# Performance work log

Hardware: AMD Instinct MI355X
Metric: run time of the kernel (lower is better)

The kernel has to match this reference:

```python
import jax, jax.numpy as jnp
import numpy as np

B, T, D, U = 16, 1600, 512, 1024


def setup_inputs() -> dict:
    key = jax.random.key(0)
    ks = jax.random.split(key, 7)
    sk = 1.0 / np.sqrt(D)
    sr = 1.0 / np.sqrt(U)
    return {
        "x": jax.random.normal(ks[0], (B, T, D), jnp.float32),
        "x_len": jnp.full((B,), T, dtype=jnp.int32),
        "kernel_f": jax.random.normal(ks[1], (D, 4 * U), jnp.float32) * sk,
        "rkernel_f": jax.random.normal(ks[2], (U, 4 * U), jnp.float32) * sr,
        "bias_f": jnp.zeros((4 * U,), jnp.float32),
        "kernel_b": jax.random.normal(ks[3], (D, 4 * U), jnp.float32) * sk,
        "rkernel_b": jax.random.normal(ks[4], (U, 4 * U), jnp.float32) * sr,
        "bias_b": jnp.zeros((4 * U,), jnp.float32),
    }


def _lstm(x, kernel, rkernel, bias):
    """Keras-semantics LSTM, return_sequences=True. x: [B,T,D] -> [B,T,U]."""
    units = rkernel.shape[0]
    # precompute input projection for all timesteps (the big GEMM)
    xg = jnp.einsum('btd,dg->btg', x, kernel) + bias  # [B,T,4U]
    xg = jnp.swapaxes(xg, 0, 1)  # [T,B,4U] for scan
    h0 = jnp.zeros((x.shape[0], units), x.dtype)
    c0 = jnp.zeros((x.shape[0], units), x.dtype)

    def step(carry, g_in):
        h, c = carry
        g = g_in + h @ rkernel  # [B,4U]
        i, f, cc, o = jnp.split(g, 4, axis=-1)  # Keras gate order i,f,c,o
        c = jax.nn.sigmoid(f) * c + jax.nn.sigmoid(i) * jnp.tanh(cc)
        h = jax.nn.sigmoid(o) * jnp.tanh(c)
        return (h, c), h

    _, hs = jax.lax.scan(step, (h0, c0), xg)  # hs: [T,B,U]
    return jnp.swapaxes(hs, 0, 1)


def reference(x, x_len, kernel_f, rkernel_f, bias_f, kernel_b, rkernel_b, bias_b):
    # Bidirectional(LSTM(units, return_sequences=True)), merge_mode='concat'
    out_f = _lstm(x, kernel_f, rkernel_f, bias_f)
    out_b = _lstm(x[:, ::-1], kernel_b, rkernel_b, bias_b)[:, ::-1]
    outputs = jnp.concatenate([out_f, out_b], axis=-1)  # [B,T,2U]
    return outputs, x_len
```

## Files before the change

kernel.cpp:

```cpp
#include <hip/hip_runtime.h>

#define B_   16
#define T_   1600
#define D_   512
#define U_   1024
#define G_   4096
#define NWG  256
#define TPB  256
#define KTOT 1536
#define APAD 1544
#define ROWB (APAD*2)
#define X16OFF (1 << 18)

typedef __attribute__((ext_vector_type(8))) __bf16 bf16x8;
typedef __attribute__((ext_vector_type(4))) float  f32x4;
typedef __attribute__((ext_vector_type(2))) float  f32x2;
typedef __attribute__((ext_vector_type(8))) unsigned short us8v;
typedef unsigned long long u64;

__device__ __forceinline__ unsigned short f2bf(float f) {
  unsigned u = __builtin_bit_cast(unsigned, f);
  u += 0x7FFFu + ((u >> 16) & 1u);
  return (unsigned short)(u >> 16);
}
__device__ __forceinline__ bf16x8 cvt8(const float4 a, const float4 b) {
  us8v r;
  r[0]=f2bf(a.x); r[1]=f2bf(a.y); r[2]=f2bf(a.z); r[3]=f2bf(a.w);
  r[4]=f2bf(b.x); r[5]=f2bf(b.y); r[6]=f2bf(b.z); r[7]=f2bf(b.w);
  return __builtin_bit_cast(bf16x8, r);
}
__device__ __forceinline__ float sigm(float x){ return 1.f / (1.f + __expf(-x)); }
__device__ __forceinline__ float tanh_(float x){ return 1.f - 2.f / (__expf(2.f*x) + 1.f); }

extern "C" __global__ void __launch_bounds__(256)
xcvt_kernel(const float* __restrict__ xin, unsigned short* __restrict__ x16) {
  const size_t i = ((size_t)blockIdx.x*256 + threadIdx.x) * 8;
  float4 a = *(const float4*)(xin + i);
  float4 b = *(const float4*)(xin + i + 4);
  *(us8v*)(x16 + i) = __builtin_bit_cast(us8v, cvt8(a, b));
}

extern "C" __global__ void __launch_bounds__(TPB, 1)
bilstm_kernel(const float* __restrict__ x, const int* __restrict__ xlen,
              const float* __restrict__ kf, const float* __restrict__ rkf, const float* __restrict__ bf_,
              const float* __restrict__ kb, const float* __restrict__ rkb, const float* __restrict__ bb_,
              float* __restrict__ out, unsigned* __restrict__ flags,
              unsigned short* __restrict__ hbuf,
              const unsigned short* __restrict__ x16, int use16)
{
  extern __shared__ char smem[];

  const int tid = threadIdx.x;
  const int wg  = blockIdx.x;
  const int dir = wg >> 7;
  const int slot = wg & 127;
  const int u0  = slot << 3;

  if (wg == 0 && tid < B_)
    out[(size_t)B_*T_*2*U_ + tid] = (float)xlen[tid];

  const float* Km = dir ? kb  : kf;
  const float* Rm = dir ? rkb : rkf;
  const float* Bv = dir ? bb_ : bf_;

  const int w = tid >> 6, l = tid & 63;
  const int ntile = w & 1, khalf = w >> 1;

  {
    char* Wb = smem;
    for (int i = tid; i < KTOT*32; i += TPB) {
      int k = i >> 5, c = i & 31;
      int gc = ((c >> 3) << 10) + u0 + (c & 7);
      float wv = (k < D_) ? Km[(size_t)k*G_ + gc] : Rm[(size_t)(k-D_)*G_ + gc];
      *(unsigned short*)(Wb + c*ROWB + (k << 1)) = f2bf(wv);
    }
  }
  __syncthreads();

  bf16x8 wx[8], wh[16];
  {
    const char* Brow = smem + (ntile*16 + (l & 15))*ROWB + ((l >> 4) << 4);
    #pragma unroll
    for (int i = 0; i < 8; ++i)  wx[i] = *(const bf16x8*)(Brow + ((khalf*8 + i) << 6));
    #pragma unroll
    for (int i = 0; i < 16; ++i) wh[i] = *(const bf16x8*)(Brow + ((16 + khalf*16 + i) << 6));
  }
  __syncthreads();

  float* gates = (float*)smem;
  char*  hst   = smem + 4096;
  float* gp    = gates + khalf*512;
  const int drow0 = (l >> 4) << 2, dcol = ntile*16 + (l & 15);

  const int eb = tid >> 2, eup = (tid & 3) << 1;
  float bi0=0, bi1=0, bff0=0, bff1=0, bz0=0, bz1=0, bo0=0, bo1=0, c0=0, c1=0;
  if (tid < 64) {
    bi0 = Bv[u0+eup];        bi1 = Bv[u0+eup+1];
    bff0= Bv[1024+u0+eup];   bff1= Bv[1024+u0+eup+1];
    bz0 = Bv[2048+u0+eup];   bz1 = Bv[2048+u0+eup+1];
    bo0 = Bv[3072+u0+eup];   bo1 = Bv[3072+u0+eup+1];
  }

  unsigned* myflags = flags + dir*128;

  const float* xbase = x + (size_t)(l & 15)*T_*D_ + khalf*256 + ((l >> 4) << 3);
  const unsigned short* x16b = x16 + (size_t)(l & 15)*T_*D_ + khalf*256 + ((l >> 4) << 3);

  const char* hrow  = hst + (l & 15)*2048;
  const int   kbase = (khalf*512 + ((l >> 4) << 3)) << 1;
  const int   swz   = ((l & 15) & 7) << 4;

  f32x4 acc = {0.f, 0.f, 0.f, 0.f};
  {
    const int tg0 = dir ? (T_ - 1) : 0;
    if (use16) {
      const unsigned short* xA = x16b + (size_t)tg0 * D_;
      #pragma unroll
      for (int i = 0; i < 8; ++i)
        acc = __builtin_amdgcn_mfma_f32_16x16x32_bf16(*(const bf16x8*)(xA + i*32), wx[i], acc, 0, 0, 0);
    } else {
      const float* xA = xbase + (size_t)tg0 * D_;
      #pragma unroll
      for (int i = 0; i < 8; ++i) {
        float4 lo = *(const float4*)(xA + i*32);
        float4 hi = *(const float4*)(xA + i*32 + 4);
        acc = __builtin_amdgcn_mfma_f32_16x16x32_bf16(cvt8(lo, hi), wx[i], acc, 0, 0, 0);
      }
    }
  }

  for (int t = 0; t < T_; ++t) {
    const int tg = dir ? (T_ - 1 - t) : t;

    if (t > 0) {
      {
        const unsigned tgt = (unsigned)t;
        long long guard = 0;
        while (__hip_atomic_load(myflags + (tid >> 1), __ATOMIC_RELAXED, __HIP_MEMORY_SCOPE_AGENT) < tgt) {
          __builtin_amdgcn_s_sleep(1);
          if (++guard > (1LL << 22)) break;
        }
      }
      {
        const u64* hsrc = (const u64*)(hbuf + (((size_t)((t & 1)*2 + dir)) << 14));
        u64 tmp[16];
        #pragma unroll
        for (int j = 0; j < 16; ++j)
          tmp[j] = __hip_atomic_load(hsrc + tid + j*256, __ATOMIC_RELAXED, __HIP_MEMORY_SCOPE_AGENT);
        #pragma unroll
        for (int j = 0; j < 16; ++j)
          *(u64*)(hst + j*2048 + ((tid << 3) ^ ((j & 7) << 4))) = tmp[j];
      }
      __syncthreads();

      f32x4 acc2 = {0.f, 0.f, 0.f, 0.f};
      #pragma unroll
      for (int i = 0; i < 16; i += 2) {
        bf16x8 a0 = *(const bf16x8*)(hrow + ((kbase + i*64)     ^ swz));
        bf16x8 a1 = *(const bf16x8*)(hrow + ((kbase + (i+1)*64) ^ swz));
        acc  = __builtin_amdgcn_mfma_f32_16x16x32_bf16(a0, wh[i],   acc,  0, 0, 0);
        acc2 = __builtin_amdgcn_mfma_f32_16x16x32_bf16(a1, wh[i+1], acc2, 0, 0, 0);
      }
      acc[0]+=acc2[0]; acc[1]+=acc2[1]; acc[2]+=acc2[2]; acc[3]+=acc2[3];
    }

    #pragma unroll
    for (int j = 0; j < 4; ++j) gp[(drow0 + j)*32 + dcol] = acc[j];
    __syncthreads();

    if (tid < 64) {
      const float* g0 = gates + eb*32 + eup;
      float gi0 = g0[0]  + g0[512] + bi0,  gi1 = g0[1]  + g0[513] + bi1;
      float gf0 = g0[8]  + g0[520] + bff0, gf1 = g0[9]  + g0[521] + bff1;
      float gz0 = g0[16] + g0[528] + bz0,  gz1 = g0[17] + g0[529] + bz1;
      float go0 = g0[24] + g0[536] + bo0,  go1 = g0[25] + g0[537] + bo1;
      c0 = sigm(gf0)*c0 + sigm(gi0)*tanh_(gz0);
      c1 = sigm(gf1)*c1 + sigm(gi1)*tanh_(gz1);
      float h0 = sigm(go0)*tanh_(c0);
      float h1 = sigm(go1)*tanh_(c1);
      unsigned hp = ((unsigned)f2bf(h1) << 16) | (unsigned)f2bf(h0);
      unsigned* hdst = (unsigned*)(hbuf + (((size_t)(((t & 1) ^ 1)*2 + dir)) << 14) + (eb << 10) + u0 + eup);
      __hip_atomic_store(hdst, hp, __ATOMIC_RELAXED, __HIP_MEMORY_SCOPE_AGENT);
      asm volatile("s_waitcnt vmcnt(0)" ::: "memory");
      if (tid == 0)
        __hip_atomic_store(myflags + slot, (unsigned)(t + 1), __ATOMIC_RELAXED, __HIP_MEMORY_SCOPE_AGENT);
      f32x2 ho; ho.x = h0; ho.y = h1;
      *(f32x2*)(out + ((size_t)eb*T_ + tg)*(2*U_) + (dir << 10) + u0 + eup) = ho;
    }

    if (t + 1 < T_) {
      const int tg1 = dir ? (T_ - 2 - t) : (t + 1);
      f32x4 nacc = {0.f, 0.f, 0.f, 0.f};
      if (use16) {
        const unsigned short* xA = x16b + (size_t)tg1 * D_;
        #pragma unroll
        for (int i = 0; i < 8; ++i)
          nacc = __builtin_amdgcn_mfma_f32_16x16x32_bf16(*(const bf16x8*)(xA + i*32), wx[i], nacc, 0, 0, 0);
      } else {
        const float* xA = xbase + (size_t)tg1 * D_;
        #pragma unroll
        for (int i = 0; i < 8; ++i) {
          float4 lo = *(const float4*)(xA + i*32);
          float4 hi = *(const float4*)(xA + i*32 + 4);
          nacc = __builtin_amdgcn_mfma_f32_16x16x32_bf16(cvt8(lo, hi), wx[i], nacc, 0, 0, 0);
        }
      }
      acc = nacc;
    }
  }
}

extern "C" void kernel_launch(void* const* d_in, const int* in_sizes, int n_in,
                              void* d_out, int out_size, void* d_ws, size_t ws_size,
                              hipStream_t stream) {
  const float* x   = (const float*)d_in[0];
  const int*   xl  = (const int*)d_in[1];
  const float* kf  = (const float*)d_in[2];
  const float* rkf = (const float*)d_in[3];
  const float* bf_ = (const float*)d_in[4];
  const float* kb  = (const float*)d_in[5];
  const float* rkb = (const float*)d_in[6];
  const float* bb_ = (const float*)d_in[7];
  float* out = (float*)d_out;

  unsigned* flags = (unsigned*)d_ws;
  unsigned short* hbuf = (unsigned short*)((char*)d_ws + 1024);
  unsigned short* x16  = (unsigned short*)((char*)d_ws + X16OFF);

  const size_t need = (size_t)X16OFF + (size_t)B_*T_*D_*2;
  const int use16 = (ws_size >= need) ? 1 : 0;

  (void)hipMemsetAsync(d_ws, 0, 1024, stream);
  if (use16)
    xcvt_kernel<<<6400, 256, 0, stream>>>(x, x16);

  const size_t smem = 32*(size_t)ROWB;
  bilstm_kernel<<<NWG, TPB, smem, stream>>>(x, xl, kf, rkf, bf_, kb, rkb, bb_,
                                            out, flags, hbuf, x16, use16);
}
```

Measured before the change: 5.343 ms.

## Replace per-step flag handshake with timestep-tagged hidden-state words

Drops the separate flag array and its spin-wait. Each hidden-state bf16 value is now stored in a 32-bit word whose upper 16 bits hold the timestep tag. Consumers poll the h buffer directly with system-coherent dwordx4 loads until every tag matches, then pack the bf16 halves into LDS. This removes the producer's store-then-wait-then-flag sequence and the consumer's flag-then-data double round trip on the serial critical path. The cost is twice the h-buffer traffic per step and a larger workspace memset.

```diff
diff --git a/kernel.cpp b/kernel.cpp
--- a/kernel.cpp
+++ b/kernel.cpp
@@ -15,8 +15,10 @@
 typedef __attribute__((ext_vector_type(8))) __bf16 bf16x8;
 typedef __attribute__((ext_vector_type(4))) float  f32x4;
 typedef __attribute__((ext_vector_type(2))) float  f32x2;
+typedef __attribute__((ext_vector_type(4))) unsigned int uint4v;
 typedef __attribute__((ext_vector_type(8))) unsigned short us8v;
 typedef unsigned long long u64;
+typedef unsigned int u32;
 
 __device__ __forceinline__ unsigned short f2bf(float f) {
   unsigned u = __builtin_bit_cast(unsigned, f);
@@ -44,8 +46,7 @@
 bilstm_kernel(const float* __restrict__ x, const int* __restrict__ xlen,
               const float* __restrict__ kf, const float* __restrict__ rkf, const float* __restrict__ bf_,
               const float* __restrict__ kb, const float* __restrict__ rkb, const float* __restrict__ bb_,
-              float* __restrict__ out, unsigned* __restrict__ flags,
-              unsigned short* __restrict__ hbuf,
+              float* __restrict__ out, u32* __restrict__ hbuf32,
               const unsigned short* __restrict__ x16, int use16)
 {
   extern __shared__ char smem[];
@@ -101,14 +102,14 @@
     bo0 = Bv[3072+u0+eup];   bo1 = Bv[3072+u0+eup+1];
   }
 
-  unsigned* myflags = flags + dir*128;
-
   const float* xbase = x + (size_t)(l & 15)*T_*D_ + khalf*256 + ((l >> 4) << 3);
   const unsigned short* x16b = x16 + (size_t)(l & 15)*T_*D_ + khalf*256 + ((l >> 4) << 3);
 
   const char* hrow  = hst + (l & 15)*2048;
   const int   kbase = (khalf*512 + ((l >> 4) << 3)) << 1;
   const int   swz   = ((l & 15) & 7) << 4;
+
+  const unsigned off0 = (unsigned)tid * 16;
 
   f32x4 acc = {0.f, 0.f, 0.f, 0.f};
   {
@@ -133,23 +134,31 @@
     const int tg = dir ? (T_ - 1 - t) : t;
 
     if (t > 0) {
-      {
-        const unsigned tgt = (unsigned)t;
-        long long guard = 0;
-        while (__hip_atomic_load(myflags + (tid >> 1), __ATOMIC_RELAXED, __HIP_MEMORY_SCOPE_AGENT) < tgt) {
-          __builtin_amdgcn_s_sleep(1);
-          if (++guard > (1LL << 22)) break;
-        }
-      }
-      {
-        const u64* hsrc = (const u64*)(hbuf + (((size_t)((t & 1)*2 + dir)) << 14));
-        u64 tmp[16];
+      const u32* hb = hbuf32 + (size_t)((t & 1)*2 + dir) * 16384;
+      const unsigned tagv = (unsigned)t << 16;
+      uint4v hv[16];
+      long long guard = 0;
+      for (;;) {
         #pragma unroll
         for (int j = 0; j < 16; ++j)
-          tmp[j] = __hip_atomic_load(hsrc + tid + j*256, __ATOMIC_RELAXED, __HIP_MEMORY_SCOPE_AGENT);
+          asm volatile("global_load_dwordx4 %0, %1, %2 sc0 sc1"
+                       : "=v"(hv[j]) : "v"(off0 + (unsigned)(j*4096)), "s"(hb));
+        asm volatile("s_waitcnt vmcnt(0)" ::: "memory");
+        __builtin_amdgcn_sched_barrier(0);
+        unsigned bad = 0;
         #pragma unroll
         for (int j = 0; j < 16; ++j)
-          *(u64*)(hst + j*2048 + ((tid << 3) ^ ((j & 7) << 4))) = tmp[j];
+          bad |= (hv[j][0] ^ tagv) | (hv[j][2] ^ tagv);
+        if (!(bad & 0xFFFF0000u)) break;
+        __builtin_amdgcn_s_sleep(1);
+        if (++guard > (1LL << 22)) break;
+      }
+      #pragma unroll
+      for (int j = 0; j < 16; ++j) {
+        u32 lo = __builtin_amdgcn_perm(hv[j][1], hv[j][0], 0x05040100u);
+        u32 hi = __builtin_amdgcn_perm(hv[j][3], hv[j][2], 0x05040100u);
+        u64 v = ((u64)hi << 32) | lo;
+        *(u64*)(hst + j*2048 + ((tid << 3) ^ ((j & 7) << 4))) = v;
       }
       __syncthreads();
 
@@ -178,12 +187,11 @@
       c1 = sigm(gf1)*c1 + sigm(gi1)*tanh_(gz1);
       float h0 = sigm(go0)*tanh_(c0);
       float h1 = sigm(go1)*tanh_(c1);
-      unsigned hp = ((unsigned)f2bf(h1) << 16) | (unsigned)f2bf(h0);
-      unsigned* hdst = (unsigned*)(hbuf + (((size_t)(((t & 1) ^ 1)*2 + dir)) << 14) + (eb << 10) + u0 + eup);
-      __hip_atomic_store(hdst, hp, __ATOMIC_RELAXED, __HIP_MEMORY_SCOPE_AGENT);
-      asm volatile("s_waitcnt vmcnt(0)" ::: "memory");
-      if (tid == 0)
-        __hip_atomic_store(myflags + slot, (unsigned)(t + 1), __ATOMIC_RELAXED, __HIP_MEMORY_SCOPE_AGENT);
+      const unsigned tagw = (unsigned)(t + 1) << 16;
+      u32 w0 = (u32)f2bf(h0) | tagw;
+      u32 w1 = (u32)f2bf(h1) | tagw;
+      u32* hdst = hbuf32 + (size_t)(((t & 1) ^ 1)*2 + dir)*16384 + (eb << 10) + u0 + eup;
+      __hip_atomic_store((u64*)hdst, ((u64)w1 << 32) | w0, __ATOMIC_RELAXED, __HIP_MEMORY_SCOPE_AGENT);
       f32x2 ho; ho.x = h0; ho.y = h1;
       *(f32x2*)(out + ((size_t)eb*T_ + tg)*(2*U_) + (dir << 10) + u0 + eup) = ho;
     }
@@ -223,18 +231,17 @@
   const float* bb_ = (const float*)d_in[7];
   float* out = (float*)d_out;
 
-  unsigned* flags = (unsigned*)d_ws;
-  unsigned short* hbuf = (unsigned short*)((char*)d_ws + 1024);
-  unsigned short* x16  = (unsigned short*)((char*)d_ws + X16OFF);
+  u32* hbuf32 = (u32*)d_ws;
+  unsigned short* x16 = (unsigned short*)((char*)d_ws + X16OFF);
 
   const size_t need = (size_t)X16OFF + (size_t)B_*T_*D_*2;
   const int use16 = (ws_size >= need) ? 1 : 0;
 
-  (void)hipMemsetAsync(d_ws, 0, 1024, stream);
+  (void)hipMemsetAsync(d_ws, 0, X16OFF, stream);
   if (use16)
     xcvt_kernel<<<6400, 256, 0, stream>>>(x, x16);
 
   const size_t smem = 32*(size_t)ROWB;
   bilstm_kernel<<<NWG, TPB, smem, stream>>>(x, xl, kf, rkf, bf_, kb, rkb, bb_,
-                                            out, flags, hbuf, x16, use16);
-}
+                                            out, hbuf32, x16, use16);
+}
```

Result: faster. 5.185 ms (median of 2 runs) (-3.0%).
